# Kernel tuning notes

Measured on AMD Instinct MI355X. Metric: run time of the kernel, lower is better.

The kernel has to match this reference:

```python
import jax, jax.numpy as jnp
import numpy as np

D_MODEL = 768
N_HEAD = 12
D_HEAD = D_MODEL // N_HEAD
B, T = 2, 2048


def setup_inputs() -> dict:
    key = jax.random.key(0)
    k1, k2, k3 = jax.random.split(key, 3)
    x = jax.random.normal(k1, (B, T, D_MODEL), dtype=jnp.float32)
    w_attn = jax.random.normal(k2, (D_MODEL, 3 * D_MODEL), dtype=jnp.float32) * (1.0 / np.sqrt(D_MODEL))
    b_attn = jnp.zeros((3 * D_MODEL,), dtype=jnp.float32)
    w_proj = jax.random.normal(k3, (D_MODEL, D_MODEL), dtype=jnp.float32) * (1.0 / np.sqrt(D_MODEL))
    b_proj = jnp.zeros((D_MODEL,), dtype=jnp.float32)
    return {"x": x, "w_attn": w_attn, "b_attn": b_attn, "w_proj": w_proj, "b_proj": b_proj}


def reference(x, w_attn, b_attn, w_proj, b_proj):
    Bq, Tq, C = x.shape
    qkv = x @ w_attn + b_attn                                  # [B, T, 3C]
    qkv = qkv.reshape(Bq, Tq, 3, N_HEAD, D_HEAD)
    q, k, v = qkv[:, :, 0], qkv[:, :, 1], qkv[:, :, 2]         # [B, T, H, Dh]
    scale = 1.0 / np.sqrt(D_HEAD)
    att = jnp.einsum('bqhd,bkhd->bhqk', q, k) * scale          # [B, H, T, T]
    causal = jnp.tril(jnp.ones((Tq, Tq), dtype=bool))
    att = jnp.where(causal[None, None], att, -jnp.inf)
    att = jax.nn.softmax(att, axis=-1)
    y = jnp.einsum('bhqk,bkhd->bqhd', att, v).reshape(Bq, Tq, C)
    return y @ w_proj + b_proj
```

## Files before the change

kernel.cpp:

```cpp
#include <hip/hip_runtime.h>
#include <hip/hip_bf16.h>

#define D_MODEL 768
#define N_HEADS 12
#define D_HEADK 64
#define BB 2
#define TT 2048
#define M_TOK (BB*TT)
#define N_QKV (3*D_MODEL)
#define MS_SEG (BB*N_HEADS*TT)

using f32x4  = __attribute__((ext_vector_type(4))) float;
using f32x16 = __attribute__((ext_vector_type(16))) float;
using s16x8  = __attribute__((ext_vector_type(8))) short;

typedef __attribute__((address_space(1))) const unsigned int ga_u32;
typedef __attribute__((address_space(3))) unsigned int ls_u32;

__device__ __forceinline__ float fast_exp2(float x) {
    return __builtin_amdgcn_exp2f(x);
}

__device__ __forceinline__ unsigned short f2bf(float f) {
    union { float f; unsigned u; } v; v.f = f;
    unsigned r = v.u + 0x7FFFu + ((v.u >> 16) & 1u);
    return (unsigned short)(r >> 16);
}

__device__ __forceinline__ float bf2f(unsigned short u) {
    union { unsigned u; float f; } v; v.u = ((unsigned)u) << 16; return v.f;
}

__device__ __forceinline__ unsigned cvtpk_bf16(float lo, float hi) {
    unsigned d;
    asm("v_cvt_pk_bf16_f32 %0, %1, %2" : "=v"(d) : "v"(lo), "v"(hi));
    return d;
}

__global__ void prep_kernel(const float* __restrict__ X, unsigned short* __restrict__ Xb,
                            const float* __restrict__ Wa, const float* __restrict__ Wp,
                            unsigned short* __restrict__ Wta, unsigned short* __restrict__ Wtp) {
    __shared__ float tile[32][33];
    const int id = blockIdx.x;
    if (id < 1536) {
        int idx = (id * 256 + threadIdx.x) * 8;
        float4 v0 = *(const float4*)&X[idx];
        float4 v1 = *(const float4*)&X[idx + 4];
        ushort4 u0, u1;
        u0.x = f2bf(v0.x); u0.y = f2bf(v0.y); u0.z = f2bf(v0.z); u0.w = f2bf(v0.w);
        u1.x = f2bf(v1.x); u1.y = f2bf(v1.y); u1.z = f2bf(v1.z); u1.w = f2bf(v1.w);
        *(ushort4*)&Xb[idx]     = u0;
        *(ushort4*)&Xb[idx + 4] = u1;
        return;
    }
    const float* W; unsigned short* Wt; int N; int j;
    if (id < 1536 + 72*24) { j = id - 1536;        W = Wa; Wt = Wta; N = N_QKV; }
    else                   { j = id - 1536 - 72*24; W = Wp; Wt = Wtp; N = D_MODEL; }
    const int nb = N / 32;
    const int bx = (j % nb) * 32;
    const int by = (j / nb) * 32;
    const int tx = threadIdx.x & 31;
    const int ty = threadIdx.x >> 5;
    #pragma unroll
    for (int i = ty; i < 32; i += 8)
        tile[i][tx] = W[(size_t)(by + i) * N + bx + tx];
    __syncthreads();
    #pragma unroll
    for (int i = ty; i < 32; i += 8)
        Wt[(size_t)(bx + i) * D_MODEL + by + tx] = f2bf(tile[tx][i]);
}

__launch_bounds__(256)
__global__ void qkv_kernel(const unsigned short* __restrict__ Xb, const unsigned short* __restrict__ Wt,
                           const float* __restrict__ bias,
                           unsigned short* __restrict__ Qw, unsigned short* __restrict__ Kw,
                           unsigned short* __restrict__ Vw) {
    __shared__ unsigned short As[128*64];
    __shared__ unsigned short Bs[128*64];
    const int m0 = blockIdx.y * 128;
    const int n0 = blockIdx.x * 128;
    const int tid = threadIdx.x;
    const int l  = tid & 63;
    const int w  = tid >> 6;
    const int wr = w >> 1, wc = w & 1;
    const int lr = l & 15, lk4 = l >> 4, li = (l >> 4) * 4;
    const int grw  = l >> 3;
    const int gslt = l & 7;

    f32x4 acc[4][4] = {};
    for (int kt = 0; kt < D_MODEL; kt += 64) {
        #pragma unroll
        for (int i = 0; i < 4; ++i) {
            const int row  = w*32 + i*8 + grw;
            const int gcol = (gslt ^ (row & 7)) << 3;
            __builtin_amdgcn_global_load_lds(
                (ga_u32*)&Xb[(size_t)(m0 + row) * D_MODEL + kt + gcol],
                (ls_u32*)&As[(w*32 + i*8) * 64], 16, 0, 0);
            __builtin_amdgcn_global_load_lds(
                (ga_u32*)&Wt[(size_t)(n0 + row) * D_MODEL + kt + gcol],
                (ls_u32*)&Bs[(w*32 + i*8) * 64], 16, 0, 0);
        }
        __syncthreads();
        #pragma unroll
        for (int ks = 0; ks < 2; ++ks) {
            s16x8 a[4], bf[4];
            #pragma unroll
            for (int mi = 0; mi < 4; ++mi) {
                const int row = wr*64 + mi*16 + lr;
                const int slot = (ks*4 + lk4) ^ (row & 7);
                a[mi] = *(const s16x8*)&As[row*64 + slot*8];
            }
            #pragma unroll
            for (int ni = 0; ni < 4; ++ni) {
                const int row = wc*64 + ni*16 + lr;
                const int slot = (ks*4 + lk4) ^ (row & 7);
                bf[ni] = *(const s16x8*)&Bs[row*64 + slot*8];
            }
            #pragma unroll
            for (int mi = 0; mi < 4; ++mi)
                #pragma unroll
                for (int ni = 0; ni < 4; ++ni)
                    acc[mi][ni] = __builtin_amdgcn_mfma_f32_16x16x32_bf16(a[mi], bf[ni], acc[mi][ni], 0, 0, 0);
        }
        __syncthreads();
    }
    #pragma unroll
    for (int ni = 0; ni < 4; ++ni) {
        int ng = n0 + wc*64 + ni*16 + lr;
        int mat = ng / D_MODEL;
        int hd  = ng % D_MODEL;
        int h = hd >> 6, d = hd & 63;
        float bv = bias[ng];
        #pragma unroll
        for (int mi = 0; mi < 4; ++mi) {
            #pragma unroll
            for (int i = 0; i < 4; ++i) {
                int t  = m0 + wr*64 + mi*16 + li + i;
                int b  = t >> 11, tq = t & 2047;
                float val = acc[mi][ni][i] + bv;
                size_t off = ((size_t)(b*N_HEADS + h)*TT + tq)*64 + d;
                if (mat == 0)      Qw[off] = f2bf(val * 0.18033688f);
                else if (mat == 1) Kw[off] = f2bf(val);
                else               Vw[off] = f2bf(val);
            }
        }
    }
}

__launch_bounds__(256)
__global__ void vtrans_kernel(const unsigned short* __restrict__ Vw, unsigned short* __restrict__ Vt) {
    __shared__ unsigned short tile[64][65];
    const int bh = blockIdx.y;
    const int t0 = blockIdx.x * 64;
    const int tid = threadIdx.x;
    const int srow = tid >> 3;
    const int scol = (tid & 7) * 8;
    const unsigned short* src = Vw + (size_t)bh * TT * 64;
    unsigned short* dst = Vt + (size_t)bh * 64 * TT;
    *(int4*)&tile[srow][scol]    = *(const int4*)&src[(size_t)(t0 + srow) * 64 + scol];
    *(int4*)&tile[srow+32][scol] = *(const int4*)&src[(size_t)(t0 + srow + 32) * 64 + scol];
    __syncthreads();
    s16x8 a0, a1;
    #pragma unroll
    for (int j = 0; j < 8; ++j) {
        a0[j] = (short)tile[scol + j][srow];
        a1[j] = (short)tile[scol + j][srow + 32];
    }
    *(s16x8*)&dst[(size_t)srow * TT + t0 + scol]        = a0;
    *(s16x8*)&dst[(size_t)(srow + 32) * TT + t0 + scol] = a1;
}

__device__ __forceinline__ int swz(int r, int c) { return r*64 + (c ^ ((r & 7) << 3)); }

__launch_bounds__(256)
__global__ void attn_kernel(const unsigned short* __restrict__ Q,
                            const unsigned short* __restrict__ Kk,
                            const unsigned short* __restrict__ Vt,
                            unsigned short* __restrict__ oA,
                            unsigned short* __restrict__ oB,
                            unsigned short* __restrict__ oC,
                            unsigned short* __restrict__ oD,
                            float* __restrict__ ms) {
    __shared__ unsigned short Ks[64*64];
    __shared__ unsigned short Vs[64*64];
    const int f   = blockIdx.y * 64 + blockIdx.x;
    const int xcd = f & 7;
    const int rr  = f >> 3;
    const int bh  = xcd * 3 + (rr % 3);
    const int px  = rr / 3;
    const int qci = 15 - (px >> 2);
    const int seg = px & 3;
    const int q0 = qci * 128;
    const int b = bh / N_HEADS, h = bh % N_HEADS;
    const int tid = threadIdx.x;
    const int l  = tid & 63;
    const int w  = tid >> 6;
    const int lq = l & 31;
    const int hi = l >> 5;
    const int srow = tid >> 3;
    const int scol = (tid & 7) * 8;
    const int qw0 = q0 + w * 32;

    const unsigned short* Qp = Q  + (size_t)bh * TT * 64;
    const unsigned short* Kp = Kk + (size_t)bh * TT * 64;
    const unsigned short* Vp = Vt + (size_t)bh * 64 * TT;

    const int ntiles  = 2 * (qci + 1);
    const int t_begin = (seg * ntiles) >> 2;
    const int t_end   = ((seg + 1) * ntiles) >> 2;

    s16x8 qsel[4];
    {
        const unsigned short* qrow = &Qp[(size_t)(qw0 + lq) * 64];
        #pragma unroll
        for (int t = 0; t < 4; ++t) {
            s16x8 qlo = *(const s16x8*)&qrow[16*t];
            s16x8 qhi = *(const s16x8*)&qrow[16*t + 8];
            qsel[t] = hi ? qhi : qlo;
        }
    }

    float mi = -1e30f, si = 0.f;
    f32x16 o0 = {}, o1 = {};

    const int kb0 = t_begin * 64;
    int4 kp0 = *(const int4*)&Kp[(size_t)(kb0 + srow) * 64 + scol];
    int4 kp1 = *(const int4*)&Kp[(size_t)(kb0 + srow + 32) * 64 + scol];
    int4 vp0 = *(const int4*)&Vp[(size_t)srow * TT + kb0 + scol];
    int4 vp1 = *(const int4*)&Vp[(size_t)(srow + 32) * TT + kb0 + scol];

    for (int it = t_begin; it < t_end; ++it) {
        const int kt = it * 64;
        __syncthreads();
        *(int4*)&Ks[swz(srow,      scol)] = kp0;
        *(int4*)&Ks[swz(srow + 32, scol)] = kp1;
        *(int4*)&Vs[swz(srow,      scol)] = vp0;
        *(int4*)&Vs[swz(srow + 32, scol)] = vp1;
        __syncthreads();
        if (it + 1 < t_end) {
            const int k2 = kt + 64;
            kp0 = *(const int4*)&Kp[(size_t)(k2 + srow) * 64 + scol];
            kp1 = *(const int4*)&Kp[(size_t)(k2 + srow + 32) * 64 + scol];
            vp0 = *(const int4*)&Vp[(size_t)srow * TT + k2 + scol];
            vp1 = *(const int4*)&Vp[(size_t)(srow + 32) * TT + k2 + scol];
        }
        #pragma unroll
        for (int kti = 0; kti < 2; ++kti) {
            const int kk = kt + kti * 32;
            if (kk > qw0) continue;
            const bool diag = (kk == qw0);
            f32x16 s = {};
            __builtin_amdgcn_s_setprio(1);
            #pragma unroll
            for (int t = 0; t < 4; ++t) {
                s16x8 a = *(const s16x8*)&Ks[swz(kti*32 + lq, 16*t + 8*hi)];
                s = __builtin_amdgcn_mfma_f32_32x32x16_bf16(a, qsel[t], s, 0, 0, 0);
            }
            __builtin_amdgcn_s_setprio(0);
            if (diag) {
                #pragma unroll
                for (int r = 0; r < 16; ++r) {
                    const int kloc = (r & 3) + 8*(r >> 2) + 4*hi;
                    if (kloc > lq) s[r] = -1e30f;
                }
            }
            float a0m = fmaxf(fmaxf(s[0],  s[1]),  s[2]);
            float a1m = fmaxf(fmaxf(s[3],  s[4]),  s[5]);
            float a2m = fmaxf(fmaxf(s[6],  s[7]),  s[8]);
            float a3m = fmaxf(fmaxf(s[9],  s[10]), s[11]);
            float a4m = fmaxf(fmaxf(s[12], s[13]), s[14]);
            float lm  = fmaxf(fmaxf(fmaxf(a0m, a1m), a2m),
                              fmaxf(fmaxf(a3m, a4m), s[15]));
            if (!__all(lm <= mi + 11.5f)) {
                float pm = fmaxf(lm, __shfl_xor(lm, 32));
                float mn = fmaxf(mi, pm);
                float sf = fast_exp2(mi - mn);
                si *= sf;
                #pragma unroll
                for (int r = 0; r < 16; ++r) {
                    const int qloc = (r & 3) + 8*(r >> 2) + 4*hi;
                    float sfq = __shfl(sf, qloc);
                    o0[r] *= sfq; o1[r] *= sfq;
                }
                mi = mn;
            }
            float e[16];
            float psum = 0.f;
            #pragma unroll
            for (int r = 0; r < 16; ++r) {
                e[r] = fast_exp2(s[r] - mi);
                psum += e[r];
            }
            si += psum;
            #pragma unroll
            for (int s2 = 0; s2 < 2; ++s2) {
                unsigned c0 = cvtpk_bf16(e[8*s2 + 0], e[8*s2 + 1]);
                unsigned c1 = cvtpk_bf16(e[8*s2 + 2], e[8*s2 + 3]);
                unsigned c2 = cvtpk_bf16(e[8*s2 + 4], e[8*s2 + 5]);
                unsigned c3 = cvtpk_bf16(e[8*s2 + 6], e[8*s2 + 7]);
                asm("v_permlane32_swap_b32 %0, %1" : "+v"(c0), "+v"(c2));
                asm("v_permlane32_swap_b32 %0, %1" : "+v"(c1), "+v"(c3));
                union { unsigned u[4]; s16x8 v; } pa;
                pa.u[0] = c0; pa.u[1] = c1; pa.u[2] = c2; pa.u[3] = c3;
                const int kc = kti*32 + 16*s2 + 8*hi;
                s16x8 vb0 = *(const s16x8*)&Vs[swz(lq,      kc)];
                s16x8 vb1 = *(const s16x8*)&Vs[swz(32 + lq, kc)];
                __builtin_amdgcn_s_setprio(1);
                o0 = __builtin_amdgcn_mfma_f32_32x32x16_bf16(pa.v, vb0, o0, 0, 0, 0);
                o1 = __builtin_amdgcn_mfma_f32_32x32x16_bf16(pa.v, vb1, o1, 0, 0, 0);
                __builtin_amdgcn_s_setprio(0);
            }
        }
    }
    float sfull = si + __shfl_xor(si, 32);
    if (hi == 0) {
        const int row = bh * TT + qw0 + lq;
        ms[seg*MS_SEG + row]       = mi;
        ms[(4+seg)*MS_SEG + row]   = sfull;
    }
    unsigned short* op = (seg == 0) ? oA : (seg == 1) ? oB : (seg == 2) ? oC : oD;
    #pragma unroll
    for (int r = 0; r < 16; ++r) {
        const int qloc = (r & 3) + 8*(r >> 2) + 4*hi;
        size_t row = (size_t)(b*TT + qw0 + qloc) * D_MODEL + h*64;
        op[row + lq]      = f2bf(o0[r]);
        op[row + 32 + lq] = f2bf(o1[r]);
    }
}

__launch_bounds__(256)
__global__ void merge_kernel(const unsigned short* __restrict__ oA,
                             const unsigned short* __restrict__ oB,
                             const unsigned short* __restrict__ oC,
                             const unsigned short* __restrict__ oD,
                             const float* __restrict__ ms,
                             unsigned short* __restrict__ Yw) {
    const int gid = blockIdx.x * 256 + threadIdx.x;
    const int e = gid * 8;
    const int t = e / D_MODEL;
    const int c = e % D_MODEL;
    const int b = t >> 11, q = t & 2047;
    const int h = c >> 6;
    const int row = (b * N_HEADS + h) * TT + q;
    float m0 = ms[row],            m1 = ms[MS_SEG + row];
    float m2 = ms[2*MS_SEG + row], m3 = ms[3*MS_SEG + row];
    float s0 = ms[4*MS_SEG + row], s1 = ms[5*MS_SEG + row];
    float s2 = ms[6*MS_SEG + row], s3 = ms[7*MS_SEG + row];
    float m  = fmaxf(fmaxf(m0, m1), fmaxf(m2, m3));
    float a0 = fast_exp2(m0 - m), a1 = fast_exp2(m1 - m);
    float a2 = fast_exp2(m2 - m), a3 = fast_exp2(m3 - m);
    float inv = 1.f / (s0*a0 + s1*a1 + s2*a2 + s3*a3);
    float w0 = a0*inv, w1 = a1*inv, w2 = a2*inv, w3 = a3*inv;
    s16x8 va = *(const s16x8*)&oA[e];
    s16x8 vb = *(const s16x8*)&oB[e];
    s16x8 vc = *(const s16x8*)&oC[e];
    s16x8 vd = *(const s16x8*)&oD[e];
    s16x8 out;
    #pragma unroll
    for (int j = 0; j < 8; ++j)
        out[j] = (short)f2bf(bf2f((unsigned short)va[j]) * w0 +
                             bf2f((unsigned short)vb[j]) * w1 +
                             bf2f((unsigned short)vc[j]) * w2 +
                             bf2f((unsigned short)vd[j]) * w3);
    *(s16x8*)&Yw[e] = out;
}

__launch_bounds__(256)
__global__ void proj_kernel(const unsigned short* __restrict__ Y, const unsigned short* __restrict__ Wt,
                            const float* __restrict__ bias, float* __restrict__ Out) {
    __shared__ unsigned short As[32][40];
    __shared__ unsigned short Bs[128][40];
    const int m0 = blockIdx.y * 32;
    const int n0 = blockIdx.x * 128;
    const int tid = threadIdx.x;
    const int l  = tid & 63;
    const int w  = tid >> 6;
    const int lr = l & 15, lk = (l >> 4) * 8, li = (l >> 4) * 4;

    f32x4 acc[2][2] = {};
    for (int kt = 0; kt < D_MODEL; kt += 32) {
        if (tid < 128) {
            int r = tid >> 2;
            int c = (tid & 3) * 8;
            *(int4*)&As[r][c] = *(const int4*)&Y[(size_t)(m0 + r) * D_MODEL + kt + c];
        }
        #pragma unroll
        for (int p = 0; p < 2; ++p) {
            int ch = tid * 2 + p;
            int r = ch >> 2;
            int c = (ch & 3) * 8;
            *(int4*)&Bs[r][c] = *(const int4*)&Wt[(size_t)(n0 + r) * D_MODEL + kt + c];
        }
        __syncthreads();
        s16x8 a[2], bf[2];
        a[0] = *(const s16x8*)&As[lr][lk];
        a[1] = *(const s16x8*)&As[16 + lr][lk];
        bf[0] = *(const s16x8*)&Bs[w*32 + lr][lk];
        bf[1] = *(const s16x8*)&Bs[w*32 + 16 + lr][lk];
        #pragma unroll
        for (int mi2 = 0; mi2 < 2; ++mi2)
            #pragma unroll
            for (int ni = 0; ni < 2; ++ni)
                acc[mi2][ni] = __builtin_amdgcn_mfma_f32_16x16x32_bf16(a[mi2], bf[ni], acc[mi2][ni], 0, 0, 0);
        __syncthreads();
    }
    #pragma unroll
    for (int ni = 0; ni < 2; ++ni) {
        int ng = n0 + w*32 + ni*16 + lr;
        float bv = bias[ng];
        #pragma unroll
        for (int mi2 = 0; mi2 < 2; ++mi2)
            #pragma unroll
            for (int i = 0; i < 4; ++i) {
                int t = m0 + mi2*16 + li + i;
                Out[(size_t)t * D_MODEL + ng] = acc[mi2][ni][i] + bv;
            }
    }
}

extern "C" void kernel_launch(void* const* d_in, const int* in_sizes, int n_in,
                              void* d_out, int out_size, void* d_ws, size_t ws_size,
                              hipStream_t stream) {
    const float* x      = (const float*)d_in[0];
    const float* w_attn = (const float*)d_in[1];
    const float* b_attn = (const float*)d_in[2];
    const float* w_proj = (const float*)d_in[3];
    const float* b_proj = (const float*)d_in[4];
    float* out = (float*)d_out;

    unsigned short* wt_attn = (unsigned short*)d_ws;
    unsigned short* wt_proj = wt_attn + (size_t)N_QKV * D_MODEL;
    unsigned short* Qw      = wt_proj + (size_t)D_MODEL * D_MODEL;
    unsigned short* Kw      = Qw + (size_t)M_TOK * D_MODEL;
    unsigned short* Vw      = Kw + (size_t)M_TOK * D_MODEL;
    unsigned short* Yw      = Vw + (size_t)M_TOK * D_MODEL;
    unsigned short* Xb      = Yw + (size_t)M_TOK * D_MODEL;
    unsigned short* oC      = Xb + (size_t)M_TOK * D_MODEL;
    unsigned short* oD      = oC + (size_t)M_TOK * D_MODEL;
    unsigned short* Vtw     = Xb;
    unsigned short* oA      = Vw;
    unsigned short* oB      = Yw;
    float*          msbuf   = (float*)d_ws;

    hipLaunchKernelGGL(prep_kernel, dim3(1536 + 72*24 + 24*24), dim3(256), 0, stream,
                       x, Xb, w_attn, w_proj, wt_attn, wt_proj);
    hipLaunchKernelGGL(qkv_kernel, dim3(N_QKV/128, M_TOK/128), dim3(256), 0, stream,
                       Xb, wt_attn, b_attn, Qw, Kw, Vw);
    hipLaunchKernelGGL(vtrans_kernel, dim3(TT/64, BB*N_HEADS), dim3(256), 0, stream,
                       Vw, Vtw);
    hipLaunchKernelGGL(attn_kernel, dim3(64, BB*N_HEADS), dim3(256), 0, stream,
                       Qw, Kw, Vtw, oA, oB, oC, oD, msbuf);
    hipLaunchKernelGGL(merge_kernel, dim3(M_TOK*D_MODEL/8/256), dim3(256), 0, stream,
                       oA, oB, oC, oD, msbuf, Yw);
    hipLaunchKernelGGL(proj_kernel, dim3(D_MODEL/128, M_TOK/32), dim3(256), 0, stream,
                       Yw, wt_proj, b_proj, out);
}
```

Measured before the change: 181.4 us.

## Fuse split-merge into projection GEMM and double-buffer attention K/V LDS tiles

The separate merge kernel is removed. The projection GEMM now reads the four partial attention outputs and the max/sum statistics directly, and combines them while staging its A tile. This drops one launch and the write/read round trip of the merged Y buffer. In exchange, every one of the six N-column blocks recomputes the merge for its rows, so partial-output reads and exp work grow several-fold. Separately, the attention kernel ping-pongs between two K/V LDS buffers, which removes one __syncthreads per key tile.

```diff
diff --git a/kernel.cpp b/kernel.cpp
--- a/kernel.cpp
+++ b/kernel.cpp
@@ -181,8 +181,8 @@
                             unsigned short* __restrict__ oC,
                             unsigned short* __restrict__ oD,
                             float* __restrict__ ms) {
-    __shared__ unsigned short Ks[64*64];
-    __shared__ unsigned short Vs[64*64];
+    __shared__ unsigned short Ks[2*64*64];
+    __shared__ unsigned short Vs[2*64*64];
     const int f   = blockIdx.y * 64 + blockIdx.x;
     const int xcd = f & 7;
     const int rr  = f >> 3;
@@ -231,11 +231,12 @@
 
     for (int it = t_begin; it < t_end; ++it) {
         const int kt = it * 64;
-        __syncthreads();
-        *(int4*)&Ks[swz(srow,      scol)] = kp0;
-        *(int4*)&Ks[swz(srow + 32, scol)] = kp1;
-        *(int4*)&Vs[swz(srow,      scol)] = vp0;
-        *(int4*)&Vs[swz(srow + 32, scol)] = vp1;
+        unsigned short* Kb = &Ks[((it - t_begin) & 1) * 4096];
+        unsigned short* Vb = &Vs[((it - t_begin) & 1) * 4096];
+        *(int4*)&Kb[swz(srow,      scol)] = kp0;
+        *(int4*)&Kb[swz(srow + 32, scol)] = kp1;
+        *(int4*)&Vb[swz(srow,      scol)] = vp0;
+        *(int4*)&Vb[swz(srow + 32, scol)] = vp1;
         __syncthreads();
         if (it + 1 < t_end) {
             const int k2 = kt + 64;
@@ -253,7 +254,7 @@
             __builtin_amdgcn_s_setprio(1);
             #pragma unroll
             for (int t = 0; t < 4; ++t) {
-                s16x8 a = *(const s16x8*)&Ks[swz(kti*32 + lq, 16*t + 8*hi)];
+                s16x8 a = *(const s16x8*)&Kb[swz(kti*32 + lq, 16*t + 8*hi)];
                 s = __builtin_amdgcn_mfma_f32_32x32x16_bf16(a, qsel[t], s, 0, 0, 0);
             }
             __builtin_amdgcn_s_setprio(0);
@@ -303,8 +304,8 @@
                 union { unsigned u[4]; s16x8 v; } pa;
                 pa.u[0] = c0; pa.u[1] = c1; pa.u[2] = c2; pa.u[3] = c3;
                 const int kc = kti*32 + 16*s2 + 8*hi;
-                s16x8 vb0 = *(const s16x8*)&Vs[swz(lq,      kc)];
-                s16x8 vb1 = *(const s16x8*)&Vs[swz(32 + lq, kc)];
+                s16x8 vb0 = *(const s16x8*)&Vb[swz(lq,      kc)];
+                s16x8 vb1 = *(const s16x8*)&Vb[swz(32 + lq, kc)];
                 __builtin_amdgcn_s_setprio(1);
                 o0 = __builtin_amdgcn_mfma_f32_32x32x16_bf16(pa.v, vb0, o0, 0, 0, 0);
                 o1 = __builtin_amdgcn_mfma_f32_32x32x16_bf16(pa.v, vb1, o1, 0, 0, 0);
@@ -329,44 +330,12 @@
 }
 
 __launch_bounds__(256)
-__global__ void merge_kernel(const unsigned short* __restrict__ oA,
-                             const unsigned short* __restrict__ oB,
-                             const unsigned short* __restrict__ oC,
-                             const unsigned short* __restrict__ oD,
-                             const float* __restrict__ ms,
-                             unsigned short* __restrict__ Yw) {
-    const int gid = blockIdx.x * 256 + threadIdx.x;
-    const int e = gid * 8;
-    const int t = e / D_MODEL;
-    const int c = e % D_MODEL;
-    const int b = t >> 11, q = t & 2047;
-    const int h = c >> 6;
-    const int row = (b * N_HEADS + h) * TT + q;
-    float m0 = ms[row],            m1 = ms[MS_SEG + row];
-    float m2 = ms[2*MS_SEG + row], m3 = ms[3*MS_SEG + row];
-    float s0 = ms[4*MS_SEG + row], s1 = ms[5*MS_SEG + row];
-    float s2 = ms[6*MS_SEG + row], s3 = ms[7*MS_SEG + row];
-    float m  = fmaxf(fmaxf(m0, m1), fmaxf(m2, m3));
-    float a0 = fast_exp2(m0 - m), a1 = fast_exp2(m1 - m);
-    float a2 = fast_exp2(m2 - m), a3 = fast_exp2(m3 - m);
-    float inv = 1.f / (s0*a0 + s1*a1 + s2*a2 + s3*a3);
-    float w0 = a0*inv, w1 = a1*inv, w2 = a2*inv, w3 = a3*inv;
-    s16x8 va = *(const s16x8*)&oA[e];
-    s16x8 vb = *(const s16x8*)&oB[e];
-    s16x8 vc = *(const s16x8*)&oC[e];
-    s16x8 vd = *(const s16x8*)&oD[e];
-    s16x8 out;
-    #pragma unroll
-    for (int j = 0; j < 8; ++j)
-        out[j] = (short)f2bf(bf2f((unsigned short)va[j]) * w0 +
-                             bf2f((unsigned short)vb[j]) * w1 +
-                             bf2f((unsigned short)vc[j]) * w2 +
-                             bf2f((unsigned short)vd[j]) * w3);
-    *(s16x8*)&Yw[e] = out;
-}
-
-__launch_bounds__(256)
-__global__ void proj_kernel(const unsigned short* __restrict__ Y, const unsigned short* __restrict__ Wt,
+__global__ void proj_kernel(const unsigned short* __restrict__ oA,
+                            const unsigned short* __restrict__ oB,
+                            const unsigned short* __restrict__ oC,
+                            const unsigned short* __restrict__ oD,
+                            const float* __restrict__ ms,
+                            const unsigned short* __restrict__ Wt,
                             const float* __restrict__ bias, float* __restrict__ Out) {
     __shared__ unsigned short As[32][40];
     __shared__ unsigned short Bs[128][40];
@@ -377,19 +346,48 @@
     const int w  = tid >> 6;
     const int lr = l & 15, lk = (l >> 4) * 8, li = (l >> 4) * 4;
 
+    const int r  = tid >> 2;
+    const int cc = (tid & 3) * 8;
+    const int t  = m0 + r;
+    const int bq = t >> 11, qq = t & 2047;
+    float w0 = 0.f, w1 = 0.f, w2 = 0.f, w3 = 0.f;
+
     f32x4 acc[2][2] = {};
     for (int kt = 0; kt < D_MODEL; kt += 32) {
         if (tid < 128) {
-            int r = tid >> 2;
-            int c = (tid & 3) * 8;
-            *(int4*)&As[r][c] = *(const int4*)&Y[(size_t)(m0 + r) * D_MODEL + kt + c];
+            if ((kt & 63) == 0) {
+                const int head = kt >> 6;
+                const int msrow = (bq * N_HEADS + head) * TT + qq;
+                float m0_ = ms[msrow],            m1_ = ms[MS_SEG + msrow];
+                float m2_ = ms[2*MS_SEG + msrow], m3_ = ms[3*MS_SEG + msrow];
+                float s0_ = ms[4*MS_SEG + msrow], s1_ = ms[5*MS_SEG + msrow];
+                float s2_ = ms[6*MS_SEG + msrow], s3_ = ms[7*MS_SEG + msrow];
+                float mm = fmaxf(fmaxf(m0_, m1_), fmaxf(m2_, m3_));
+                float a0 = fast_exp2(m0_ - mm), a1 = fast_exp2(m1_ - mm);
+                float a2 = fast_exp2(m2_ - mm), a3 = fast_exp2(m3_ - mm);
+                float inv = 1.f / (s0_*a0 + s1_*a1 + s2_*a2 + s3_*a3);
+                w0 = a0*inv; w1 = a1*inv; w2 = a2*inv; w3 = a3*inv;
+            }
+            size_t e = (size_t)t * D_MODEL + kt + cc;
+            s16x8 va = *(const s16x8*)&oA[e];
+            s16x8 vb = *(const s16x8*)&oB[e];
+            s16x8 vc = *(const s16x8*)&oC[e];
+            s16x8 vd = *(const s16x8*)&oD[e];
+            s16x8 mg;
+            #pragma unroll
+            for (int j = 0; j < 8; ++j)
+                mg[j] = (short)f2bf(bf2f((unsigned short)va[j]) * w0 +
+                                    bf2f((unsigned short)vb[j]) * w1 +
+                                    bf2f((unsigned short)vc[j]) * w2 +
+                                    bf2f((unsigned short)vd[j]) * w3);
+            *(s16x8*)&As[r][cc] = mg;
         }
         #pragma unroll
         for (int p = 0; p < 2; ++p) {
             int ch = tid * 2 + p;
-            int r = ch >> 2;
-            int c = (ch & 3) * 8;
-            *(int4*)&Bs[r][c] = *(const int4*)&Wt[(size_t)(n0 + r) * D_MODEL + kt + c];
+            int rb = ch >> 2;
+            int cb = (ch & 3) * 8;
+            *(int4*)&Bs[rb][cb] = *(const int4*)&Wt[(size_t)(n0 + rb) * D_MODEL + kt + cb];
         }
         __syncthreads();
         s16x8 a[2], bf[2];
@@ -412,8 +410,8 @@
         for (int mi2 = 0; mi2 < 2; ++mi2)
             #pragma unroll
             for (int i = 0; i < 4; ++i) {
-                int t = m0 + mi2*16 + li + i;
-                Out[(size_t)t * D_MODEL + ng] = acc[mi2][ni][i] + bv;
+                int tt = m0 + mi2*16 + li + i;
+                Out[(size_t)tt * D_MODEL + ng] = acc[mi2][ni][i] + bv;
             }
     }
 }
@@ -450,8 +448,6 @@
                        Vw, Vtw);
     hipLaunchKernelGGL(attn_kernel, dim3(64, BB*N_HEADS), dim3(256), 0, stream,
                        Qw, Kw, Vtw, oA, oB, oC, oD, msbuf);
-    hipLaunchKernelGGL(merge_kernel, dim3(M_TOK*D_MODEL/8/256), dim3(256), 0, stream,
-                       oA, oB, oC, oD, msbuf, Yw);
     hipLaunchKernelGGL(proj_kernel, dim3(D_MODEL/128, M_TOK/32), dim3(256), 0, stream,
-                       Yw, wt_proj, b_proj, out);
-}
+                       oA, oB, oC, oD, msbuf, wt_proj, b_proj, out);
+}
```

New measurement: 188.9 us. 4.1% more time.
